# Kernel optimization log

Measured on AMD Instinct MI355X. Metric: run time of the kernel, lower is better.

Reference implementation:

```python
import jax, jax.numpy as jnp
import numpy as np

NUM_HEADS = 12
EMBED_DIM = 768
HEAD_DIM = EMBED_DIM // NUM_HEADS


def _rope_cos_sin():
    # Faithful to source: RoPE is applied with seq_dim=1 on [b,h,n,d] tensors,
    # so the "position" axis is actually the HEAD axis (length NUM_HEADS).
    inv_freq = 1.0 / (10000.0 ** (jnp.arange(0, HEAD_DIM, 2, dtype=jnp.float32) / HEAD_DIM))
    t = jnp.arange(NUM_HEADS, dtype=jnp.float32)
    freqs = t[:, None] * inv_freq[None, :]            # [H, D/2]
    emb = jnp.concatenate([freqs, freqs], axis=-1)     # [H, D]
    cos = jnp.cos(emb)[None, :, None, :]               # [1, H, 1, D] broadcasts over seq
    sin = jnp.sin(emb)[None, :, None, :]
    return cos, sin


def _apply_rope(x, cos, sin):
    # x: [B, H, N, D]
    x1, x2 = jnp.split(x, 2, axis=-1)
    x_rot = jnp.concatenate([-x2, x1], axis=-1)
    return x * cos + x_rot * sin


def setup_inputs() -> dict:
    key = jax.random.key(0)
    k1, k2, k3, k4, k5 = jax.random.split(key, 5)
    B, N, E = 8, 1024, EMBED_DIM
    s_in = 1.0 / np.sqrt(E)
    return {
        "x": jax.random.normal(k1, (B, N, E), dtype=jnp.float32),
        "w_qkv": jax.random.uniform(k2, (E, 3 * E), dtype=jnp.float32, minval=-s_in, maxval=s_in),
        "b_qkv": jax.random.uniform(k3, (3 * E,), dtype=jnp.float32, minval=-s_in, maxval=s_in),
        "w_proj": jax.random.uniform(k4, (E, E), dtype=jnp.float32, minval=-s_in, maxval=s_in),
        "b_proj": jax.random.uniform(k5, (E,), dtype=jnp.float32, minval=-s_in, maxval=s_in),
    }


def reference(x, w_qkv, b_qkv, w_proj, b_proj):
    B, N, E = x.shape
    H, D = NUM_HEADS, HEAD_DIM
    scale = D ** (-0.5)

    qkv = x @ w_qkv + b_qkv                                  # [B, N, 3E]
    qkv = qkv.reshape(B, N, 3, H, D).transpose(2, 0, 3, 1, 4)  # [3, B, H, N, D]
    q, k, v = qkv[0], qkv[1], qkv[2]

    cos, sin = _rope_cos_sin()
    q = _apply_rope(q, cos, sin)
    k = _apply_rope(k, cos, sin)

    attn = jnp.einsum('bhid,bhjd->bhij', q, k) * scale       # [B, H, N, N]
    attn = jax.nn.softmax(attn, axis=-1)
    out = jnp.einsum('bhij,bhjd->bhid', attn, v)             # [B, H, N, D]
    out = out.transpose(0, 2, 1, 3).reshape(B, N, E)         # [B, N, E]
    return out @ w_proj + b_proj
```

## Files before the change

kernel.cpp:

```cpp
#include <hip/hip_runtime.h>
#include <math.h>

#define NH 12
#define HD 64
#define NSEQ 1024
#define BATCH 8
#define EMB 768
#define NQKV 2304
#define MROWS 8192

typedef _Float16 half8 __attribute__((ext_vector_type(8)));
typedef _Float16 half4 __attribute__((ext_vector_type(4)));
typedef _Float16 half2v __attribute__((ext_vector_type(2)));
typedef float f32x4 __attribute__((ext_vector_type(4)));
typedef float f32x16 __attribute__((ext_vector_type(16)));
typedef unsigned int u32;

#define MFMA16(a,b,c) __builtin_amdgcn_mfma_f32_16x16x32_f16(a, b, c, 0, 0, 0)
#define MFMA32(a,b,c) __builtin_amdgcn_mfma_f32_32x32x16_f16(a, b, c, 0, 0, 0)

#define QSCALE 0.18033688011112043f
#define EXPB 5.770780163555856f

#define ASYNC16(g, l)                                                          \
  __builtin_amdgcn_global_load_lds(                                            \
      (const __attribute__((address_space(1))) unsigned int*)(g),              \
      (__attribute__((address_space(3))) unsigned int*)(l), 16, 0, 0)

__device__ __forceinline__ void transpose_tile(const float* __restrict__ in,
                                               _Float16* __restrict__ out,
                                               int R, int C, int bx, int by,
                                               _Float16 (*T)[72]) {
  const int tr = by * 64, tc = bx * 64;
  const int r = threadIdx.x >> 2, s = threadIdx.x & 3;
  const float* src = in + (size_t)(tr + r) * C + tc + s * 16;
  _Float16* dst = &T[r][s * 16];
  #pragma unroll
  for (int i = 0; i < 4; ++i) {
    float4 v = ((const float4*)src)[i];
    dst[4*i+0] = (_Float16)v.x; dst[4*i+1] = (_Float16)v.y;
    dst[4*i+2] = (_Float16)v.z; dst[4*i+3] = (_Float16)v.w;
  }
  __syncthreads();
  alignas(16) _Float16 tmp[16];
  #pragma unroll
  for (int j = 0; j < 16; ++j) tmp[j] = T[s * 16 + j][r];
  half8* o = (half8*)(out + (size_t)(tc + r) * R + tr + s * 16);
  o[0] = *(half8*)&tmp[0];
  o[1] = *(half8*)&tmp[8];
}

__global__ __launch_bounds__(256) void prepass(const float* __restrict__ x,
                                               _Float16* __restrict__ xh,
                                               const float* __restrict__ wq,
                                               _Float16* __restrict__ wqT,
                                               const float* __restrict__ wp,
                                               _Float16* __restrict__ wpT) {
  __shared__ _Float16 T[64][72];
  const int bid = blockIdx.x;
  if (bid < 6144) {
    int i = bid * 256 + threadIdx.x;
    float4 v = ((const float4*)x)[i];
    half4 h = { (_Float16)v.x, (_Float16)v.y, (_Float16)v.z, (_Float16)v.w };
    ((half4*)xh)[i] = h;
  } else if (bid < 6576) {
    int idx = bid - 6144;
    transpose_tile(wq, wqT, EMB, NQKV, idx % 36, idx / 36, T);
  } else {
    int idx = bid - 6576;
    transpose_tile(wp, wpT, EMB, EMB, idx % 12, idx / 12, T);
  }
}

__device__ __forceinline__ int xcd_remap() {
  const int flat = blockIdx.y * gridDim.x + blockIdx.x;
  const int q = (gridDim.x * gridDim.y) >> 3;
  return (flat & 7) * q + (flat >> 3);
}

template<int MODE>
__global__ __launch_bounds__(256) void gemm_mfma(const _Float16* __restrict__ A,
                                                 const _Float16* __restrict__ BT,
                                                 const float* __restrict__ bias,
                                                 float* __restrict__ outf,
                                                 _Float16* __restrict__ qo,
                                                 _Float16* __restrict__ ko,
                                                 _Float16* __restrict__ vo,
                                                 int K) {
  const int BUFH = 128 * 32;
  __shared__ __align__(16) _Float16 As[2 * 128 * 32];
  __shared__ __align__(16) _Float16 Bs[2 * 128 * 32];
  const int tid = threadIdx.x;
  const int lane = tid & 63, wave = tid >> 6;
  const int quad = lane >> 4, l15 = lane & 15;
  const int wm = (wave >> 1) * 64, wn = (wave & 1) * 64;
  const int nf = xcd_remap();
  const int row0 = (nf / gridDim.x) * 128, col0 = (nf % gridDim.x) * 128;

  const int srow = lane >> 2;
  const int sseg = (lane & 3) ^ ((srow >> 1) & 3);
  const _Float16* gA = A + (size_t)(row0 + wave*32 + srow) * K + sseg * 8;
  const _Float16* gB = BT + (size_t)(col0 + wave*32 + srow) * K + sseg * 8;
  _Float16* lA = As + (wave * 32) * 32;
  _Float16* lB = Bs + (wave * 32) * 32;

  const int xq = (quad ^ ((l15 >> 1) & 3)) * 8;

  f32x4 acc[4][4];
  #pragma unroll
  for (int i = 0; i < 4; ++i)
    #pragma unroll
    for (int j = 0; j < 4; ++j) {
      f32x4 z = {0.f, 0.f, 0.f, 0.f};
      acc[i][j] = z;
    }

  ASYNC16(gA,          lA);
  ASYNC16(gA + 16 * K, lA + 16*32);
  ASYNC16(gB,          lB);
  ASYNC16(gB + 16 * K, lB + 16*32);
  __syncthreads();

  int buf = 0;
  for (int k0 = 0; k0 < K; k0 += 32) {
    if (k0 + 32 < K) {
      const int nb = (buf ^ 1) * BUFH;
      ASYNC16(gA + k0 + 32,          lA + nb);
      ASYNC16(gA + k0 + 32 + 16 * K, lA + nb + 16*32);
      ASYNC16(gB + k0 + 32,          lB + nb);
      ASYNC16(gB + k0 + 32 + 16 * K, lB + nb + 16*32);
    }
    const _Float16* Ab = As + buf * BUFH;
    const _Float16* Bb = Bs + buf * BUFH;
    half8 af[4], bf[4];
    #pragma unroll
    for (int mt = 0; mt < 4; ++mt)
      af[mt] = *(const half8*)(Ab + (wm + mt*16 + l15) * 32 + xq);
    #pragma unroll
    for (int nt = 0; nt < 4; ++nt)
      bf[nt] = *(const half8*)(Bb + (wn + nt*16 + l15) * 32 + xq);
    #pragma unroll
    for (int mt = 0; mt < 4; ++mt)
      #pragma unroll
      for (int nt = 0; nt < 4; ++nt)
        acc[mt][nt] = MFMA16(af[mt], bf[nt], acc[mt][nt]);
    __syncthreads();
    buf ^= 1;
  }

  float bcol[4];
  #pragma unroll
  for (int nt = 0; nt < 4; ++nt)
    bcol[nt] = bias[col0 + wn + nt*16 + l15];

  if (MODE == 0) {
    const int ch = col0 + wn;
    const int tt = ch / EMB;
    const int hh = (ch % EMB) >> 6;
    float cs[2], sn[2];
    if (tt < 2) {
      #pragma unroll
      for (int j = 0; j < 2; ++j) {
        float fi = (float)(j*16 + l15);
        float ang = (float)hh * expf(-0.28782313662425574f * fi);
        sincosf(ang, &sn[j], &cs[j]);
      }
    }
    #pragma unroll
    for (int mt = 0; mt < 4; ++mt) {
      int m0 = row0 + wm + mt*16 + quad*4;
      int b = m0 >> 10, n0 = m0 & 1023;
      size_t bh = (size_t)(b * NH + hh);
      if (tt == 2) {
        int np = (n0 & ~12) | ((n0 & 4) << 1) | ((n0 & 8) >> 1);
        #pragma unroll
        for (int nt = 0; nt < 4; ++nt) {
          int d = nt*16 + l15;
          half4 pk;
          #pragma unroll
          for (int r = 0; r < 4; ++r)
            pk[r] = (_Float16)(acc[mt][nt][r] + bcol[nt]);
          *(half4*)(vo + (bh * HD + d) * NSEQ + np) = pk;
        }
      } else {
        _Float16* dst = (tt == 0) ? qo : ko;
        const float sc = (tt == 0) ? QSCALE : 1.0f;
        #pragma unroll
        for (int j = 0; j < 2; ++j) {
          #pragma unroll
          for (int r = 0; r < 4; ++r) {
            float lo = acc[mt][j][r]     + bcol[j];
            float hi = acc[mt][j + 2][r] + bcol[j + 2];
            float nlo = (lo * cs[j] - hi * sn[j]) * sc;
            float nhi = (hi * cs[j] + lo * sn[j]) * sc;
            size_t rowoff = (bh * NSEQ + (size_t)(n0 + r)) * HD;
            dst[rowoff + j*16 + l15]      = (_Float16)nlo;
            dst[rowoff + j*16 + l15 + 32] = (_Float16)nhi;
          }
        }
      }
    }
  } else {
    #pragma unroll
    for (int mt = 0; mt < 4; ++mt) {
      int m0 = row0 + wm + mt*16 + quad*4;
      #pragma unroll
      for (int nt = 0; nt < 4; ++nt)
        #pragma unroll
        for (int r = 0; r < 4; ++r)
          outf[(size_t)(m0 + r) * EMB + col0 + wn + nt*16 + l15] =
              acc[mt][nt][r] + bcol[nt];
    }
  }
}

__global__ __launch_bounds__(256) void attn_mfma32(const _Float16* __restrict__ q,
                                                   const _Float16* __restrict__ k,
                                                   const _Float16* __restrict__ vt,
                                                   _Float16* __restrict__ ao) {
  const int BUFH = 64 * 64;
  __shared__ __align__(16) _Float16 Ks[2 * 64 * 64];
  __shared__ __align__(16) _Float16 Vs[2 * 64 * 64];
  const int tid = threadIdx.x;
  const int lane = tid & 63, wave = tid >> 6;
  const int l31 = lane & 31, hi = lane >> 5;
  const int nf = xcd_remap();
  const int bh = nf >> 3;
  const int qrow = (nf & 7) * 128 + wave * 32 + l31;
  const size_t base = (size_t)bh * NSEQ * HD;

  const _Float16* qp = q + base + (size_t)qrow * HD + hi * 8;
  half8 qf[4];
  #pragma unroll
  for (int kh = 0; kh < 4; ++kh)
    qf[kh] = *(const half8*)(qp + kh * 16);

  const int srow8 = lane >> 3;
  const int sseg8 = lane & 7;
  const int wseg8 = sseg8 ^ (srow8 & 7);
  const _Float16* kg = k + base + (size_t)(wave*16 + srow8) * HD + sseg8 * 8;
  const _Float16* vg = vt + (size_t)bh * HD * NSEQ
                       + (size_t)(wave*16 + srow8) * NSEQ + sseg8 * 8;
  _Float16* wK0 = Ks + (wave*16 + srow8) * 64 + wseg8 * 8;
  _Float16* wV0 = Vs + (wave*16 + srow8) * 64 + wseg8 * 8;

  int xofs[4];
  #pragma unroll
  for (int kh = 0; kh < 4; ++kh)
    xofs[kh] = ((kh*2 + hi) ^ (l31 & 7)) * 8;

  f32x16 O[2];
  #pragma unroll
  for (int dt = 0; dt < 2; ++dt)
    #pragma unroll
    for (int r = 0; r < 16; ++r) O[dt][r] = 0.f;
  float l = 0.f;

  half8 rk0 = *(const half8*)(kg);
  half8 rk1 = *(const half8*)(kg + 8 * HD);
  half8 rv0 = *(const half8*)(vg);
  half8 rv1 = *(const half8*)(vg + 8 * NSEQ);
  *(half8*)(wK0)          = rk0;
  *(half8*)(wK0 + 8*64)   = rk1;
  *(half8*)(wV0)          = rv0;
  *(half8*)(wV0 + 8*64)   = rv1;
  __syncthreads();

  int buf = 0;
  for (int c0 = 0; c0 < NSEQ; c0 += 64) {
    const bool more = (c0 + 64 < NSEQ);
    if (more) {
      rk0 = *(const half8*)(kg + (size_t)(c0 + 64) * HD);
      rk1 = *(const half8*)(kg + (size_t)(c0 + 72) * HD);
      rv0 = *(const half8*)(vg + c0 + 64);
      rv1 = *(const half8*)(vg + 8 * NSEQ + c0 + 64);
    }
    const _Float16* Kb = Ks + buf * BUFH;
    const _Float16* Vb = Vs + buf * BUFH;

    f32x16 ct[2];
    __builtin_amdgcn_s_setprio(1);
    #pragma unroll
    for (int kt = 0; kt < 2; ++kt) {
      #pragma unroll
      for (int r = 0; r < 16; ++r) ct[kt][r] = 0.f;
      #pragma unroll
      for (int kh = 0; kh < 4; ++kh) {
        half8 kf = *(const half8*)(Kb + (kt*32 + l31) * 64 + xofs[kh]);
        ct[kt] = MFMA32(kf, qf[kh], ct[kt]);
      }
    }
    __builtin_amdgcn_s_setprio(0);

    union { half2v v; int i; } ph2[16];
    float rs = 0.f;
    #pragma unroll
    for (int kt = 0; kt < 2; ++kt)
      #pragma unroll
      for (int rp = 0; rp < 8; ++rp) {
        float p0 = __builtin_amdgcn_exp2f(ct[kt][2*rp]     - EXPB);
        float p1 = __builtin_amdgcn_exp2f(ct[kt][2*rp + 1] - EXPB);
        rs += p0 + p1;
        half2v hp = { (_Float16)p0, (_Float16)p1 };
        ph2[kt*8 + rp].v = hp;
      }
    l += rs;

    __builtin_amdgcn_s_setprio(1);
    #pragma unroll
    for (int kh = 0; kh < 4; ++kh) {
      const int kt = kh >> 1;
      const int iA = kt*8 + (kh & 1)*4;
      union { half8 h; int d[4]; } pf;
      pf.d[0] = ph2[iA].i;     pf.d[1] = ph2[iA + 1].i;
      pf.d[2] = ph2[iA + 2].i; pf.d[3] = ph2[iA + 3].i;
      #pragma unroll
      for (int dt = 0; dt < 2; ++dt) {
        half8 vf = *(const half8*)(Vb + (dt*32 + l31) * 64 + xofs[kh]);
        O[dt] = MFMA32(vf, pf.h, O[dt]);
      }
    }
    __builtin_amdgcn_s_setprio(0);

    if (more) {
      const int nb = (buf ^ 1) * BUFH;
      *(half8*)(wK0 + nb)        = rk0;
      *(half8*)(wK0 + nb + 8*64) = rk1;
      *(half8*)(wV0 + nb)        = rv0;
      *(half8*)(wV0 + nb + 8*64) = rv1;
    }
    __syncthreads();
    buf ^= 1;
  }

  l += __shfl_xor(l, 32);

  const int b = bh / NH, hh = bh % NH;
  const float inv = 1.0f / l;
  _Float16* orow = ao + (size_t)(b * NSEQ + qrow) * EMB + hh * HD;
  #pragma unroll
  for (int dt = 0; dt < 2; ++dt)
    #pragma unroll
    for (int t = 0; t < 4; ++t) {
      int d0 = dt*32 + 8*t + 4*hi;
      half4 o4;
      #pragma unroll
      for (int j = 0; j < 4; ++j)
        o4[j] = (_Float16)(O[dt][4*t + j] * inv);
      *(half4*)(orow + d0) = o4;
    }
}

extern "C" void kernel_launch(void* const* d_in, const int* in_sizes, int n_in,
                              void* d_out, int out_size, void* d_ws, size_t ws_size,
                              hipStream_t stream) {
  const float* x      = (const float*)d_in[0];
  const float* w_qkv  = (const float*)d_in[1];
  const float* b_qkv  = (const float*)d_in[2];
  const float* w_proj = (const float*)d_in[3];
  const float* b_proj = (const float*)d_in[4];
  float* out = (float*)d_out;

  _Float16* xh  = (_Float16*)d_ws;
  _Float16* wqT = xh  + (size_t)MROWS * EMB;
  _Float16* wpT = wqT + (size_t)NQKV * EMB;
  _Float16* qh  = wpT + (size_t)EMB * EMB;
  _Float16* kh  = qh  + (size_t)BATCH*NH*NSEQ*HD;
  _Float16* vth = kh  + (size_t)BATCH*NH*NSEQ*HD;
  _Float16* aoh = vth + (size_t)BATCH*NH*NSEQ*HD;

  prepass<<<6720, 256, 0, stream>>>(x, xh, w_qkv, wqT, w_proj, wpT);

  gemm_mfma<0><<<dim3(NQKV/128, MROWS/128), 256, 0, stream>>>(
      xh, wqT, b_qkv, nullptr, qh, kh, vth, EMB);

  attn_mfma32<<<dim3(NSEQ/128, BATCH*NH), 256, 0, stream>>>(qh, kh, vth, aoh);

  gemm_mfma<1><<<dim3(EMB/128, MROWS/128), 256, 0, stream>>>(
      aoh, wpT, b_proj, out, nullptr, nullptr, nullptr, EMB);
}
```

Measured before the change: 199.4 us.

## Use async global-to-LDS loads in attention and narrow projection GEMM tiles

The attention kernel now stages K and V tiles with direct async global-to-LDS copies, moving the XOR swizzle to the global read address. This replaces the register round trip and the explicit LDS stores after compute. The output projection GEMM gets its own kernel with 128x64 tiles, which doubles the grid from 384 to 768 blocks so more CUs are occupied. The cost is a smaller per-wave tile (4x2 MFMAs) with less data reuse per block.

```diff
diff --git a/kernel.cpp b/kernel.cpp
--- a/kernel.cpp
+++ b/kernel.cpp
@@ -78,15 +78,13 @@
   return (flat & 7) * q + (flat >> 3);
 }
 
-template<int MODE>
-__global__ __launch_bounds__(256) void gemm_mfma(const _Float16* __restrict__ A,
-                                                 const _Float16* __restrict__ BT,
-                                                 const float* __restrict__ bias,
-                                                 float* __restrict__ outf,
-                                                 _Float16* __restrict__ qo,
-                                                 _Float16* __restrict__ ko,
-                                                 _Float16* __restrict__ vo,
-                                                 int K) {
+__global__ __launch_bounds__(256) void gemm_qkv(const _Float16* __restrict__ A,
+                                                const _Float16* __restrict__ BT,
+                                                const float* __restrict__ bias,
+                                                _Float16* __restrict__ qo,
+                                                _Float16* __restrict__ ko,
+                                                _Float16* __restrict__ vo,
+                                                int K) {
   const int BUFH = 128 * 32;
   __shared__ __align__(16) _Float16 As[2 * 128 * 32];
   __shared__ __align__(16) _Float16 Bs[2 * 128 * 32];
@@ -153,64 +151,130 @@
   for (int nt = 0; nt < 4; ++nt)
     bcol[nt] = bias[col0 + wn + nt*16 + l15];
 
-  if (MODE == 0) {
-    const int ch = col0 + wn;
-    const int tt = ch / EMB;
-    const int hh = (ch % EMB) >> 6;
-    float cs[2], sn[2];
-    if (tt < 2) {
+  const int ch = col0 + wn;
+  const int tt = ch / EMB;
+  const int hh = (ch % EMB) >> 6;
+  float cs[2], sn[2];
+  if (tt < 2) {
+    #pragma unroll
+    for (int j = 0; j < 2; ++j) {
+      float fi = (float)(j*16 + l15);
+      float ang = (float)hh * expf(-0.28782313662425574f * fi);
+      sincosf(ang, &sn[j], &cs[j]);
+    }
+  }
+  #pragma unroll
+  for (int mt = 0; mt < 4; ++mt) {
+    int m0 = row0 + wm + mt*16 + quad*4;
+    int b = m0 >> 10, n0 = m0 & 1023;
+    size_t bh = (size_t)(b * NH + hh);
+    if (tt == 2) {
+      int np = (n0 & ~12) | ((n0 & 4) << 1) | ((n0 & 8) >> 1);
+      #pragma unroll
+      for (int nt = 0; nt < 4; ++nt) {
+        int d = nt*16 + l15;
+        half4 pk;
+        #pragma unroll
+        for (int r = 0; r < 4; ++r)
+          pk[r] = (_Float16)(acc[mt][nt][r] + bcol[nt]);
+        *(half4*)(vo + (bh * HD + d) * NSEQ + np) = pk;
+      }
+    } else {
+      _Float16* dst = (tt == 0) ? qo : ko;
+      const float sc = (tt == 0) ? QSCALE : 1.0f;
       #pragma unroll
       for (int j = 0; j < 2; ++j) {
-        float fi = (float)(j*16 + l15);
-        float ang = (float)hh * expf(-0.28782313662425574f * fi);
-        sincosf(ang, &sn[j], &cs[j]);
-      }
-    }
-    #pragma unroll
-    for (int mt = 0; mt < 4; ++mt) {
-      int m0 = row0 + wm + mt*16 + quad*4;
-      int b = m0 >> 10, n0 = m0 & 1023;
-      size_t bh = (size_t)(b * NH + hh);
-      if (tt == 2) {
-        int np = (n0 & ~12) | ((n0 & 4) << 1) | ((n0 & 8) >> 1);
         #pragma unroll
-        for (int nt = 0; nt < 4; ++nt) {
-          int d = nt*16 + l15;
-          half4 pk;
-          #pragma unroll
-          for (int r = 0; r < 4; ++r)
-            pk[r] = (_Float16)(acc[mt][nt][r] + bcol[nt]);
-          *(half4*)(vo + (bh * HD + d) * NSEQ + np) = pk;
-        }
-      } else {
-        _Float16* dst = (tt == 0) ? qo : ko;
-        const float sc = (tt == 0) ? QSCALE : 1.0f;
-        #pragma unroll
-        for (int j = 0; j < 2; ++j) {
-          #pragma unroll
-          for (int r = 0; r < 4; ++r) {
-            float lo = acc[mt][j][r]     + bcol[j];
-            float hi = acc[mt][j + 2][r] + bcol[j + 2];
-            float nlo = (lo * cs[j] - hi * sn[j]) * sc;
-            float nhi = (hi * cs[j] + lo * sn[j]) * sc;
-            size_t rowoff = (bh * NSEQ + (size_t)(n0 + r)) * HD;
-            dst[rowoff + j*16 + l15]      = (_Float16)nlo;
-            dst[rowoff + j*16 + l15 + 32] = (_Float16)nhi;
-          }
+        for (int r = 0; r < 4; ++r) {
+          float lo = acc[mt][j][r]     + bcol[j];
+          float hi = acc[mt][j + 2][r] + bcol[j + 2];
+          float nlo = (lo * cs[j] - hi * sn[j]) * sc;
+          float nhi = (hi * cs[j] + lo * sn[j]) * sc;
+          size_t rowoff = (bh * NSEQ + (size_t)(n0 + r)) * HD;
+          dst[rowoff + j*16 + l15]      = (_Float16)nlo;
+          dst[rowoff + j*16 + l15 + 32] = (_Float16)nhi;
         }
       }
     }
-  } else {
-    #pragma unroll
-    for (int mt = 0; mt < 4; ++mt) {
-      int m0 = row0 + wm + mt*16 + quad*4;
-      #pragma unroll
-      for (int nt = 0; nt < 4; ++nt)
-        #pragma unroll
-        for (int r = 0; r < 4; ++r)
-          outf[(size_t)(m0 + r) * EMB + col0 + wn + nt*16 + l15] =
-              acc[mt][nt][r] + bcol[nt];
-    }
+  }
+}
+
+__global__ __launch_bounds__(256) void gemm_proj(const _Float16* __restrict__ A,
+                                                 const _Float16* __restrict__ BT,
+                                                 const float* __restrict__ bias,
+                                                 float* __restrict__ outf,
+                                                 int K) {
+  const int ABUF = 128 * 32, BBUF = 64 * 32;
+  __shared__ __align__(16) _Float16 As[2 * ABUF];
+  __shared__ __align__(16) _Float16 Bs[2 * BBUF];
+  const int tid = threadIdx.x;
+  const int lane = tid & 63, wave = tid >> 6;
+  const int quad = lane >> 4, l15 = lane & 15;
+  const int wm = (wave >> 1) * 64, wn = (wave & 1) * 32;
+  const int nf = xcd_remap();
+  const int row0 = (nf / gridDim.x) * 128, col0 = (nf % gridDim.x) * 64;
+
+  const int srow = lane >> 2;
+  const int sseg = (lane & 3) ^ ((srow >> 1) & 3);
+  const _Float16* gA = A  + (size_t)(row0 + wave*32 + srow) * K + sseg * 8;
+  const _Float16* gB = BT + (size_t)(col0 + wave*16 + srow) * K + sseg * 8;
+  _Float16* lA = As + (wave * 32) * 32;
+  _Float16* lB = Bs + (wave * 16) * 32;
+
+  const int xq = (quad ^ ((l15 >> 1) & 3)) * 8;
+
+  f32x4 acc[4][2];
+  #pragma unroll
+  for (int i = 0; i < 4; ++i)
+    #pragma unroll
+    for (int j = 0; j < 2; ++j) {
+      f32x4 z = {0.f, 0.f, 0.f, 0.f};
+      acc[i][j] = z;
+    }
+
+  ASYNC16(gA,          lA);
+  ASYNC16(gA + 16 * K, lA + 16*32);
+  ASYNC16(gB,          lB);
+  __syncthreads();
+
+  int buf = 0;
+  for (int k0 = 0; k0 < K; k0 += 32) {
+    if (k0 + 32 < K) {
+      ASYNC16(gA + k0 + 32,          lA + (buf ^ 1) * ABUF);
+      ASYNC16(gA + k0 + 32 + 16 * K, lA + (buf ^ 1) * ABUF + 16*32);
+      ASYNC16(gB + k0 + 32,          lB + (buf ^ 1) * BBUF);
+    }
+    const _Float16* Ab = As + buf * ABUF;
+    const _Float16* Bb = Bs + buf * BBUF;
+    half8 af[4], bf[2];
+    #pragma unroll
+    for (int mt = 0; mt < 4; ++mt)
+      af[mt] = *(const half8*)(Ab + (wm + mt*16 + l15) * 32 + xq);
+    #pragma unroll
+    for (int nt = 0; nt < 2; ++nt)
+      bf[nt] = *(const half8*)(Bb + (wn + nt*16 + l15) * 32 + xq);
+    #pragma unroll
+    for (int mt = 0; mt < 4; ++mt)
+      #pragma unroll
+      for (int nt = 0; nt < 2; ++nt)
+        acc[mt][nt] = MFMA16(af[mt], bf[nt], acc[mt][nt]);
+    __syncthreads();
+    buf ^= 1;
+  }
+
+  float bcol[2];
+  #pragma unroll
+  for (int nt = 0; nt < 2; ++nt)
+    bcol[nt] = bias[col0 + wn + nt*16 + l15];
+  #pragma unroll
+  for (int mt = 0; mt < 4; ++mt) {
+    int m0 = row0 + wm + mt*16 + quad*4;
+    #pragma unroll
+    for (int nt = 0; nt < 2; ++nt)
+      #pragma unroll
+      for (int r = 0; r < 4; ++r)
+        outf[(size_t)(m0 + r) * EMB + col0 + wn + nt*16 + l15] =
+            acc[mt][nt][r] + bcol[nt];
   }
 }
 
@@ -238,11 +302,11 @@
   const int srow8 = lane >> 3;
   const int sseg8 = lane & 7;
   const int wseg8 = sseg8 ^ (srow8 & 7);
-  const _Float16* kg = k + base + (size_t)(wave*16 + srow8) * HD + sseg8 * 8;
+  const _Float16* kg = k + base + (size_t)(wave*16 + srow8) * HD + wseg8 * 8;
   const _Float16* vg = vt + (size_t)bh * HD * NSEQ
-                       + (size_t)(wave*16 + srow8) * NSEQ + sseg8 * 8;
-  _Float16* wK0 = Ks + (wave*16 + srow8) * 64 + wseg8 * 8;
-  _Float16* wV0 = Vs + (wave*16 + srow8) * 64 + wseg8 * 8;
+                       + (size_t)(wave*16 + srow8) * NSEQ + wseg8 * 8;
+  _Float16* uK = Ks + (wave * 16) * 64;
+  _Float16* uV = Vs + (wave * 16) * 64;
 
   int xofs[4];
   #pragma unroll
@@ -256,24 +320,21 @@
     for (int r = 0; r < 16; ++r) O[dt][r] = 0.f;
   float l = 0.f;
 
-  half8 rk0 = *(const half8*)(kg);
-  half8 rk1 = *(const half8*)(kg + 8 * HD);
-  half8 rv0 = *(const half8*)(vg);
-  half8 rv1 = *(const half8*)(vg + 8 * NSEQ);
-  *(half8*)(wK0)          = rk0;
-  *(half8*)(wK0 + 8*64)   = rk1;
-  *(half8*)(wV0)          = rv0;
-  *(half8*)(wV0 + 8*64)   = rv1;
+  ASYNC16(kg,              uK);
+  ASYNC16(kg + 8 * HD,     uK + 8*64);
+  ASYNC16(vg,              uV);
+  ASYNC16(vg + 8 * NSEQ,   uV + 8*64);
   __syncthreads();
 
   int buf = 0;
   for (int c0 = 0; c0 < NSEQ; c0 += 64) {
-    const bool more = (c0 + 64 < NSEQ);
-    if (more) {
-      rk0 = *(const half8*)(kg + (size_t)(c0 + 64) * HD);
-      rk1 = *(const half8*)(kg + (size_t)(c0 + 72) * HD);
-      rv0 = *(const half8*)(vg + c0 + 64);
-      rv1 = *(const half8*)(vg + 8 * NSEQ + c0 + 64);
+    if (c0 + 64 < NSEQ) {
+      const int nb = (buf ^ 1) * BUFH;
+      const _Float16* kc = kg + (size_t)(c0 + 64) * HD;
+      ASYNC16(kc,                  uK + nb);
+      ASYNC16(kc + 8 * HD,         uK + nb + 8*64);
+      ASYNC16(vg + c0 + 64,        uV + nb);
+      ASYNC16(vg + 8*NSEQ + c0 + 64, uV + nb + 8*64);
     }
     const _Float16* Kb = Ks + buf * BUFH;
     const _Float16* Vb = Vs + buf * BUFH;
@@ -322,13 +383,6 @@
     }
     __builtin_amdgcn_s_setprio(0);
 
-    if (more) {
-      const int nb = (buf ^ 1) * BUFH;
-      *(half8*)(wK0 + nb)        = rk0;
-      *(half8*)(wK0 + nb + 8*64) = rk1;
-      *(half8*)(wV0 + nb)        = rv0;
-      *(half8*)(wV0 + nb + 8*64) = rv1;
-    }
     __syncthreads();
     buf ^= 1;
   }
@@ -371,11 +425,11 @@
 
   prepass<<<6720, 256, 0, stream>>>(x, xh, w_qkv, wqT, w_proj, wpT);
 
-  gemm_mfma<0><<<dim3(NQKV/128, MROWS/128), 256, 0, stream>>>(
-      xh, wqT, b_qkv, nullptr, qh, kh, vth, EMB);
+  gemm_qkv<<<dim3(NQKV/128, MROWS/128), 256, 0, stream>>>(
+      xh, wqT, b_qkv, qh, kh, vth, EMB);
 
   attn_mfma32<<<dim3(NSEQ/128, BATCH*NH), 256, 0, stream>>>(qh, kh, vth, aoh);
 
-  gemm_mfma<1><<<dim3(EMB/128, MROWS/128), 256, 0, stream>>>(
-      aoh, wpT, b_proj, out, nullptr, nullptr, nullptr, EMB);
-}
+  gemm_proj<<<dim3(EMB/64, MROWS/128), 256, 0, stream>>>(
+      aoh, wpT, b_proj, out, EMB);
+}
```

After: 196.2 us. About the same (-1.6%).
